# Optimization experiments

Measured on AMD Instinct MI355X. Metric: run time of the kernel, lower is better.

The kernel has to match this reference:

```python
import jax, jax.numpy as jnp
import numpy as np

HEAD = 3
EMB = 192
MAX_LAYER = 4
NEG_SLOPE_ATT = 0.2
NEG_SLOPE_ACT = 0.1
BN_EPS = 1e-5

def leaky_relu(x, slope):
    return jnp.where(x >= 0, x, slope * x)

def setup_inputs() -> dict:
    key = jax.random.key(0)
    ks = jax.random.split(key, 8)
    N, E, D_IN = 64000, 512000, 128
    k = EMB // HEAD
    subx = jax.random.normal(ks[0], (N, D_IN), dtype=jnp.float32)
    edge_index = jax.random.randint(ks[1], (2, E), 0, N, dtype=jnp.int32)
    mask = jax.random.randint(ks[2], (E, 1), 0, 2, dtype=jnp.int32)
    W = jax.random.normal(ks[3], (EMB, D_IN), dtype=jnp.float32) * (1.0 / np.sqrt(D_IN))
    att = jax.random.normal(ks[4], (1, HEAD, 2 * k), dtype=jnp.float32) * 0.1
    bias = jnp.zeros((EMB,), dtype=jnp.float32)
    gamma = jnp.ones((EMB,), dtype=jnp.float32)
    beta = jnp.zeros((EMB,), dtype=jnp.float32)
    return {"subx": subx, "edge_index": edge_index, "mask": mask, "W": W,
            "att": att, "bias": bias, "gamma": gamma, "beta": beta,
            "batch_size": 32, "subgraph_size": 500}

def reference(subx, edge_index, mask, W, att, bias, gamma, beta, batch_size, subgraph_size):
    N = subx.shape[0]
    k = EMB // HEAD
    # linear projection, split into heads: [N, H, k]
    x = (subx @ W.T).reshape(N, HEAD, k)
    src = edge_index[0]  # softmax grouping index (as in original code)
    dst = edge_index[1]  # aggregation target (PyG source_to_target flow)
    x_i = x[dst]  # [E, H, k]
    x_j = x[src]  # [E, H, k]
    # attention logits per edge per head
    alpha = (jnp.concatenate([x_i, x_j], axis=-1) * att).sum(-1)  # [E, H]
    alpha = leaky_relu(alpha, NEG_SLOPE_ATT)
    # segment softmax grouped by src (faithful to original)
    amax = jax.ops.segment_max(alpha, src, num_segments=N)
    ex = jnp.exp(alpha - amax[src])
    denom = jax.ops.segment_sum(ex, src, num_segments=N)
    alpha = ex / (denom[src] + 1e-16)
    # edge mask (tile over heads)
    m = (mask.reshape(-1, 1, 1) != 0)
    msg = jnp.where(m, x_j, 0.0) * alpha[..., None]  # [E, H, k]
    # scatter-add to target nodes
    aggr = jax.ops.segment_sum(msg, dst, num_segments=N).reshape(N, EMB) + bias
    # LeakyReLU(0.1) then BatchNorm1d (training-mode batch stats)
    h = leaky_relu(aggr, NEG_SLOPE_ACT)
    mean = h.mean(axis=0)
    var = h.var(axis=0)
    h = gamma * (h - mean) / jnp.sqrt(var + BN_EPS) + beta
    # mean over k-hop layers
    h = h.reshape(batch_size, MAX_LAYER, subgraph_size, EMB)
    return h.mean(axis=1)
```

## Files before the change

### kernel.cpp

```cpp
#include <hip/hip_runtime.h>

#define EMBD 192
#define DIN 128
#define SB 1024

typedef __bf16 bfrag __attribute__((ext_vector_type(8)));
typedef float  f32x4 __attribute__((ext_vector_type(4)));

__device__ __forceinline__ void f4add(float4& a, const float4& b){
  a.x += b.x; a.y += b.y; a.z += b.z; a.w += b.w;
}
__device__ __forceinline__ unsigned short f2bf(float f){
  unsigned u = __float_as_uint(f);
  unsigned r = u + 0x7fffu + ((u >> 16) & 1u);
  return (unsigned short)(r >> 16);
}
__device__ __forceinline__ float bf2f(unsigned short h){
  return __uint_as_float(((unsigned)h) << 16);
}

__global__ __launch_bounds__(256) void k_gemm(const float* __restrict__ A,
      const float* __restrict__ W, const float* __restrict__ att,
      float* __restrict__ X, float* __restrict__ ai4, float* __restrict__ aj4,
      unsigned* __restrict__ zbuf, long zcount, int N, int G){
  {
    long i = (long)blockIdx.x*blockDim.x + threadIdx.x;
    long st = (long)gridDim.x*blockDim.x;
    for (; i < zcount; i += st) zbuf[i] = 0u;
  }

  int flat = blockIdx.x;
  int L = (G % 8 == 0) ? ((flat & 7)*(G >> 3) + (flat >> 3)) : flat;
  int rowblk = L / 3, head = L - rowblk*3;

  __shared__ unsigned short As_hi[8192], As_lo[8192];
  __shared__ unsigned short Ws_hi[8192], Ws_lo[8192];
  int t = threadIdx.x;

  const float4* Ag = (const float4*)A;
  const float4* Wg = (const float4*)W + (size_t)(head*64)*32;
  #pragma unroll
  for (int i = 0; i < 8; i++){
    int idx = i*256 + t;
    int r = idx >> 5, c4 = idx & 31;
    int g = (c4 >> 1) ^ (r & 15);
    int base = (r*16 + g)*8 + (c4 & 1)*4;
    int row = rowblk*64 + r; if (row >= N) row = N - 1;
    float4 va = Ag[(size_t)row*32 + c4];
    float4 vw = Wg[(size_t)idx];
    unsigned short h; float lo;
    ushort4 ah, al, wh, wl;
    h = f2bf(va.x); lo = va.x - bf2f(h); ah.x = h; al.x = f2bf(lo);
    h = f2bf(va.y); lo = va.y - bf2f(h); ah.y = h; al.y = f2bf(lo);
    h = f2bf(va.z); lo = va.z - bf2f(h); ah.z = h; al.z = f2bf(lo);
    h = f2bf(va.w); lo = va.w - bf2f(h); ah.w = h; al.w = f2bf(lo);
    *(ushort4*)&As_hi[base] = ah; *(ushort4*)&As_lo[base] = al;
    h = f2bf(vw.x); lo = vw.x - bf2f(h); wh.x = h; wl.x = f2bf(lo);
    h = f2bf(vw.y); lo = vw.y - bf2f(h); wh.y = h; wl.y = f2bf(lo);
    h = f2bf(vw.z); lo = vw.z - bf2f(h); wh.z = h; wl.z = f2bf(lo);
    h = f2bf(vw.w); lo = vw.w - bf2f(h); wh.w = h; wl.w = f2bf(lo);
    *(ushort4*)&Ws_hi[base] = wh; *(ushort4*)&Ws_lo[base] = wl;
  }

  int wave = t >> 6, lane = t & 63;
  int lc = lane & 15, kg = lane >> 4;
  float atti_l[4], attj_l[4];
  #pragma unroll
  for (int ct = 0; ct < 4; ct++){
    atti_l[ct] = att[head*128 + ct*16 + lc];
    attj_l[ct] = att[head*128 + 64 + ct*16 + lc];
  }
  __syncthreads();

  int arow = wave*16 + lc;
  f32x4 acc[4];
  #pragma unroll
  for (int ct = 0; ct < 4; ct++) acc[ct] = (f32x4){0.f, 0.f, 0.f, 0.f};

  #pragma unroll
  for (int ks = 0; ks < 4; ks++){
    int g = ks*4 + kg;
    int aoff = (arow*16 + (g ^ (arow & 15)))*8;
    bfrag ah = *(const bfrag*)&As_hi[aoff];
    bfrag al = *(const bfrag*)&As_lo[aoff];
    #pragma unroll
    for (int ct = 0; ct < 4; ct++){
      int boff = ((ct*16 + lc)*16 + (g ^ lc))*8;
      bfrag bh = *(const bfrag*)&Ws_hi[boff];
      bfrag bl = *(const bfrag*)&Ws_lo[boff];
      acc[ct] = __builtin_amdgcn_mfma_f32_16x16x32_bf16(ah, bh, acc[ct], 0, 0, 0);
      acc[ct] = __builtin_amdgcn_mfma_f32_16x16x32_bf16(ah, bl, acc[ct], 0, 0, 0);
      acc[ct] = __builtin_amdgcn_mfma_f32_16x16x32_bf16(al, bh, acc[ct], 0, 0, 0);
    }
  }

  int mbase = rowblk*64 + wave*16 + kg*4;
  #pragma unroll
  for (int r = 0; r < 4; r++){
    int m = mbase + r;
    bool ok = (m < N);
    float pi = 0.f, pj = 0.f;
    #pragma unroll
    for (int ct = 0; ct < 4; ct++){
      float v = acc[ct][r];
      if (ok) X[(size_t)m*EMBD + head*64 + ct*16 + lc] = v;
      pi += v*atti_l[ct]; pj += v*attj_l[ct];
    }
    pi += __shfl_xor(pi, 1); pi += __shfl_xor(pi, 2);
    pi += __shfl_xor(pi, 4); pi += __shfl_xor(pi, 8);
    pj += __shfl_xor(pj, 1); pj += __shfl_xor(pj, 2);
    pj += __shfl_xor(pj, 4); pj += __shfl_xor(pj, 8);
    if (ok && lc == 0){ ai4[(size_t)m*4 + head] = pi; aj4[(size_t)m*4 + head] = pj; }
  }
}

__global__ void k_count(const int* __restrict__ ei, const int* __restrict__ msk,
    int* __restrict__ count2, int* __restrict__ slot_src, int* __restrict__ slot_dst,
    int E, int N){
  int e = blockIdx.x*256 + threadIdx.x;
  if (e >= E) return;
  int s = ei[e], d = ei[E + e];
  slot_src[e] = atomicAdd(&count2[s], 1);
  slot_dst[e] = msk[e] ? atomicAdd(&count2[N + d], 1) : -1;
}

__global__ void k_scan1(const int* __restrict__ count, int* __restrict__ offs,
                        int* __restrict__ bsum, int M){
  __shared__ int sm[256];
  int t = threadIdx.x, i = blockIdx.x*256 + t;
  int v = (i < M) ? count[i] : 0;
  sm[t] = v; __syncthreads();
  for (int o = 1; o < 256; o <<= 1){
    int u = (t >= o) ? sm[t-o] : 0;
    __syncthreads();
    sm[t] += u;
    __syncthreads();
  }
  if (i < M) offs[i] = sm[t] - v;
  if (t == 255) bsum[blockIdx.x] = sm[255];
}

__global__ void k_scan2(int* __restrict__ bsum, int NB){
  __shared__ int sm[1024];
  int t = threadIdx.x;
  int v = (t < NB) ? bsum[t] : 0;
  sm[t] = v; __syncthreads();
  for (int o = 1; o < 1024; o <<= 1){
    int u = (t >= o) ? sm[t-o] : 0;
    __syncthreads();
    sm[t] += u;
    __syncthreads();
  }
  if (t < NB) bsum[t] = sm[t] - v;
}

__global__ void k_scan3(int* __restrict__ offs, const int* __restrict__ bsum, int M){
  int i = blockIdx.x*256 + threadIdx.x;
  if (i < M) offs[i] += bsum[blockIdx.x];
}

__global__ void k_fill(const int* __restrict__ ei, const int* __restrict__ slot_src,
    const int* __restrict__ slot_dst, const int* __restrict__ offs2,
    int* __restrict__ elist_src, int* __restrict__ elist_dst, int E, int N){
  int e = blockIdx.x*256 + threadIdx.x;
  if (e >= E) return;
  int s = ei[e], d = ei[E + e];
  elist_src[offs2[s] + slot_src[e]] = d;
  int sd = slot_dst[e];
  if (sd >= 0) elist_dst[offs2[N + d] + sd] = s;
}

__global__ __launch_bounds__(256) void k_denom(const int* __restrict__ count2,
    const int* __restrict__ offs2, const int* __restrict__ elist_src,
    const float4* __restrict__ ai4, const float4* __restrict__ aj4,
    float4* __restrict__ denom4, int N){
  int g = threadIdx.x >> 4, l = threadIdx.x & 15;
  int n = blockIdx.x*16 + g;
  if (n >= N) return;
  int deg = count2[n];
  if (deg == 0) return;
  int base = offs2[n];
  float4 xj = aj4[n];
  float s0 = 0.f, s1 = 0.f, s2 = 0.f;
  for (int j = l; j < deg; j += 16){
    int d = elist_src[base + j];
    float4 xi = ai4[d];
    float a0 = xi.x + xj.x; a0 = a0 >= 0.f ? a0 : 0.2f*a0; s0 += expf(a0);
    float a1 = xi.y + xj.y; a1 = a1 >= 0.f ? a1 : 0.2f*a1; s1 += expf(a1);
    float a2 = xi.z + xj.z; a2 = a2 >= 0.f ? a2 : 0.2f*a2; s2 += expf(a2);
  }
  s0 += __shfl_xor(s0, 1); s0 += __shfl_xor(s0, 2); s0 += __shfl_xor(s0, 4); s0 += __shfl_xor(s0, 8);
  s1 += __shfl_xor(s1, 1); s1 += __shfl_xor(s1, 2); s1 += __shfl_xor(s1, 4); s1 += __shfl_xor(s1, 8);
  s2 += __shfl_xor(s2, 1); s2 += __shfl_xor(s2, 2); s2 += __shfl_xor(s2, 4); s2 += __shfl_xor(s2, 8);
  if (l == 0)
    denom4[n] = make_float4(1.f/(s0 + 1e-16f), 1.f/(s1 + 1e-16f), 1.f/(s2 + 1e-16f), 0.f);
}

__global__ __launch_bounds__(256) void k_aggr(const float* __restrict__ X,
    const int* __restrict__ count2, const int* __restrict__ offs2,
    const int* __restrict__ elist_dst, const float4* __restrict__ ai4,
    const float4* __restrict__ aj4, const float4* __restrict__ denom4,
    const float* __restrict__ bias, float* __restrict__ hact, int N){
  int w = threadIdx.x >> 6, l = threadIdx.x & 63;
  int n = blockIdx.x*4 + w;
  if (n >= N) return;
  int deg = count2[N + n], base = offs2[N + n];
  float4 xi = ai4[n];
  float ac0 = 0.f, ac1 = 0.f, ac2 = 0.f;
  #pragma unroll 4
  for (int j = 0; j < deg; j++){
    int s = elist_dst[base + j];
    float4 xj = aj4[s];
    float4 rn = denom4[s];
    float a0 = xi.x + xj.x; a0 = a0 >= 0.f ? a0 : 0.2f*a0; float c0 = expf(a0)*rn.x;
    float a1 = xi.y + xj.y; a1 = a1 >= 0.f ? a1 : 0.2f*a1; float c1 = expf(a1)*rn.y;
    float a2 = xi.z + xj.z; a2 = a2 >= 0.f ? a2 : 0.2f*a2; float c2 = expf(a2)*rn.z;
    const float* xr = X + (size_t)s*EMBD;
    ac0 += c0 * xr[l];
    ac1 += c1 * xr[64 + l];
    ac2 += c2 * xr[128 + l];
  }
  float* o = hact + (size_t)n*EMBD;
  float v0 = ac0 + bias[l];       v0 = v0 >= 0.f ? v0 : 0.1f*v0; o[l]       = v0;
  float v1 = ac1 + bias[64 + l];  v1 = v1 >= 0.f ? v1 : 0.1f*v1; o[64 + l]  = v1;
  float v2 = ac2 + bias[128 + l]; v2 = v2 >= 0.f ? v2 : 0.1f*v2; o[128 + l] = v2;
}

__global__ __launch_bounds__(192) void k_stat1(const float4* __restrict__ h4,
    float4* __restrict__ part4, int N){
  int t = threadIdx.x;
  int fcol = t % 48, rg = t / 48;
  float4 s = make_float4(0.f,0.f,0.f,0.f);
  float4 q = make_float4(0.f,0.f,0.f,0.f);
  for (int r = blockIdx.x*4 + rg; r < N; r += SB*4){
    float4 v = h4[(size_t)r*48 + fcol];
    s.x += v.x; s.y += v.y; s.z += v.z; s.w += v.w;
    q.x += v.x*v.x; q.y += v.y*v.y; q.z += v.z*v.z; q.w += v.w*v.w;
  }
  __shared__ float4 sms[192], smq[192];
  sms[t] = s; smq[t] = q;
  __syncthreads();
  if (rg < 2){ f4add(sms[t], sms[t+96]); f4add(smq[t], smq[t+96]); }
  __syncthreads();
  if (rg == 0){
    f4add(sms[t], sms[t+48]); f4add(smq[t], smq[t+48]);
    part4[(size_t)blockIdx.x*96 + fcol]      = sms[t];
    part4[(size_t)blockIdx.x*96 + 48 + fcol] = smq[t];
  }
}

__global__ __launch_bounds__(256) void k_stat2(const float4* __restrict__ part4,
    float4* __restrict__ stats4, int N){
  int j = blockIdx.x, t = threadIdx.x;
  float4 s = make_float4(0.f,0.f,0.f,0.f);
  float4 q = make_float4(0.f,0.f,0.f,0.f);
  for (int b = t; b < SB; b += 256){
    f4add(s, part4[(size_t)b*96 + j]);
    f4add(q, part4[(size_t)b*96 + 48 + j]);
  }
  #pragma unroll
  for (int o = 32; o > 0; o >>= 1){
    s.x += __shfl_xor(s.x,o); s.y += __shfl_xor(s.y,o);
    s.z += __shfl_xor(s.z,o); s.w += __shfl_xor(s.w,o);
    q.x += __shfl_xor(q.x,o); q.y += __shfl_xor(q.y,o);
    q.z += __shfl_xor(q.z,o); q.w += __shfl_xor(q.w,o);
  }
  __shared__ float4 ws[4], wq[4];
  int wv = t >> 6;
  if ((t & 63) == 0){ ws[wv] = s; wq[wv] = q; }
  __syncthreads();
  if (t == 0){
    f4add(ws[0], ws[1]); f4add(ws[0], ws[2]); f4add(ws[0], ws[3]);
    f4add(wq[0], wq[1]); f4add(wq[0], wq[2]); f4add(wq[0], wq[3]);
    float inv = 1.f / (float)N;
    float4 mean = make_float4(ws[0].x*inv, ws[0].y*inv, ws[0].z*inv, ws[0].w*inv);
    float4 rstd;
    rstd.x = rsqrtf(wq[0].x*inv - mean.x*mean.x + 1e-5f);
    rstd.y = rsqrtf(wq[0].y*inv - mean.y*mean.y + 1e-5f);
    rstd.z = rsqrtf(wq[0].z*inv - mean.z*mean.z + 1e-5f);
    rstd.w = rsqrtf(wq[0].w*inv - mean.w*mean.w + 1e-5f);
    stats4[j] = mean;
    stats4[48 + j] = rstd;
  }
}

__global__ void k_final(const float* __restrict__ hact, const float* __restrict__ stats,
    const float* __restrict__ gamma, const float* __restrict__ beta,
    const int* __restrict__ sgs, float* __restrict__ out, int total){
  int o = blockIdx.x*256 + threadIdx.x;
  if (o >= total) return;
  int S = *sgs;
  int c  = o % EMBD;
  int rs = o / EMBD;
  int b  = rs / S;
  int s  = rs % S;
  size_t n0 = (size_t)b*4*S + s;
  float v = 0.25f * (hact[(n0      )*EMBD + c] + hact[(n0 +   S)*EMBD + c] +
                     hact[(n0 + 2*S)*EMBD + c] + hact[(n0 + 3*S)*EMBD + c]);
  out[o] = gamma[c] * ((v - stats[c]) * stats[192 + c]) + beta[c];
}

extern "C" void kernel_launch(void* const* d_in, const int* in_sizes, int n_in,
                              void* d_out, int out_size, void* d_ws, size_t ws_size,
                              hipStream_t stream){
  const float* subx  = (const float*)d_in[0];
  const int*   ei    = (const int*)d_in[1];
  const int*   msk   = (const int*)d_in[2];
  const float* W     = (const float*)d_in[3];
  const float* att   = (const float*)d_in[4];
  const float* bias  = (const float*)d_in[5];
  const float* gamma = (const float*)d_in[6];
  const float* beta  = (const float*)d_in[7];
  const int*   sgs   = (const int*)d_in[9];
  float* out = (float*)d_out;

  int N = in_sizes[0] / DIN;
  int E = in_sizes[1] / 2;

  float*  X         = (float*)d_ws;
  float*  hact      = X + (size_t)N*EMBD;
  float*  denom4    = hact + (size_t)N*EMBD;
  float*  ai4       = denom4 + (size_t)N*4;
  float*  aj4       = ai4 + (size_t)N*4;
  int*    count2    = (int*)(aj4 + (size_t)N*4);
  int*    offs2     = count2 + 2*(size_t)N;
  int*    slot_src  = offs2 + 2*(size_t)N;
  int*    slot_dst  = slot_src + E;
  int*    elist_src = slot_dst + E;
  int*    elist_dst = elist_src + E;
  int*    bsum      = elist_dst + E;
  float*  part      = (float*)(bsum + 1024);
  float*  stats     = part + (size_t)SB*96*4;

  int EB  = (E + 255)/256;
  int MB2 = (N + 63)/64;
  int G   = MB2*3;
  int M2  = 2*N;
  int NB2 = (M2 + 255)/256;

  k_gemm <<<G, 256, 0, stream>>>(subx, W, att, X, ai4, aj4,
                                 (unsigned*)count2, (long)M2, N, G);
  k_count<<<EB, 256, 0, stream>>>(ei, msk, count2, slot_src, slot_dst, E, N);
  k_scan1<<<NB2, 256, 0, stream>>>(count2, offs2, bsum, M2);
  k_scan2<<<1, 1024, 0, stream>>>(bsum, NB2);
  k_scan3<<<NB2, 256, 0, stream>>>(offs2, bsum, M2);
  k_fill <<<EB, 256, 0, stream>>>(ei, slot_src, slot_dst, offs2, elist_src, elist_dst, E, N);
  k_denom<<<(N + 15)/16, 256, 0, stream>>>(count2, offs2, elist_src,
                                           (const float4*)ai4, (const float4*)aj4,
                                           (float4*)denom4, N);
  k_aggr <<<(N + 3)/4, 256, 0, stream>>>(X, count2, offs2, elist_dst,
                                         (const float4*)ai4, (const float4*)aj4,
                                         (const float4*)denom4, bias, hact, N);
  k_stat1<<<SB, 192, 0, stream>>>((const float4*)hact, (float4*)part, N);
  k_stat2<<<48, 256, 0, stream>>>((const float4*)part, (float4*)stats, N);
  k_final<<<(out_size + 255)/256, 256, 0, stream>>>(hact, stats, gamma, beta, sgs, out, out_size);
}
```

Measured before the change: 265.3 us.

## Precompute per-edge attention coefficients and vectorize aggregation with float4 gathers

Adds a k_coef kernel that computes the normalized attention coefficient per destination-sorted edge once and packs it with the source index into a float4. k_aggr then does one float4 load per edge instead of recomputing the exponentials redundantly in all 64 lanes. It also gathers X rows as float4 with 48 active lanes. expf is replaced by __expf. The cost is an extra kernel launch plus writing and reading a 16-byte-per-edge coefficient buffer, and 16 of 64 lanes sit idle in aggregation.

```diff
diff --git a/kernel.cpp b/kernel.cpp
--- a/kernel.cpp
+++ b/kernel.cpp
@@ -140,7 +140,7 @@
   if (t == 255) bsum[blockIdx.x] = sm[255];
 }
 
-__global__ void k_scan2(int* __restrict__ bsum, int NB){
+__global__ void k_scan2(int* __restrict__ bsum, int* __restrict__ gtot, int NB){
   __shared__ int sm[1024];
   int t = threadIdx.x;
   int v = (t < NB) ? bsum[t] : 0;
@@ -152,6 +152,7 @@
     __syncthreads();
   }
   if (t < NB) bsum[t] = sm[t] - v;
+  if (t == NB-1) *gtot = sm[t];
 }
 
 __global__ void k_scan3(int* __restrict__ offs, const int* __restrict__ bsum, int M){
@@ -161,13 +162,13 @@
 
 __global__ void k_fill(const int* __restrict__ ei, const int* __restrict__ slot_src,
     const int* __restrict__ slot_dst, const int* __restrict__ offs2,
-    int* __restrict__ elist_src, int* __restrict__ elist_dst, int E, int N){
+    int* __restrict__ elist_src, int2* __restrict__ pairs_dst, int E, int N){
   int e = blockIdx.x*256 + threadIdx.x;
   if (e >= E) return;
   int s = ei[e], d = ei[E + e];
   elist_src[offs2[s] + slot_src[e]] = d;
   int sd = slot_dst[e];
-  if (sd >= 0) elist_dst[offs2[N + d] + sd] = s;
+  if (sd >= 0) pairs_dst[offs2[N + d] + sd - E] = make_int2(s, d);
 }
 
 __global__ __launch_bounds__(256) void k_denom(const int* __restrict__ count2,
@@ -185,9 +186,9 @@
   for (int j = l; j < deg; j += 16){
     int d = elist_src[base + j];
     float4 xi = ai4[d];
-    float a0 = xi.x + xj.x; a0 = a0 >= 0.f ? a0 : 0.2f*a0; s0 += expf(a0);
-    float a1 = xi.y + xj.y; a1 = a1 >= 0.f ? a1 : 0.2f*a1; s1 += expf(a1);
-    float a2 = xi.z + xj.z; a2 = a2 >= 0.f ? a2 : 0.2f*a2; s2 += expf(a2);
+    float a0 = xi.x + xj.x; a0 = a0 >= 0.f ? a0 : 0.2f*a0; s0 += __expf(a0);
+    float a1 = xi.y + xj.y; a1 = a1 >= 0.f ? a1 : 0.2f*a1; s1 += __expf(a1);
+    float a2 = xi.z + xj.z; a2 = a2 >= 0.f ? a2 : 0.2f*a2; s2 += __expf(a2);
   }
   s0 += __shfl_xor(s0, 1); s0 += __shfl_xor(s0, 2); s0 += __shfl_xor(s0, 4); s0 += __shfl_xor(s0, 8);
   s1 += __shfl_xor(s1, 1); s1 += __shfl_xor(s1, 2); s1 += __shfl_xor(s1, 4); s1 += __shfl_xor(s1, 8);
@@ -196,34 +197,51 @@
     denom4[n] = make_float4(1.f/(s0 + 1e-16f), 1.f/(s1 + 1e-16f), 1.f/(s2 + 1e-16f), 0.f);
 }
 
-__global__ __launch_bounds__(256) void k_aggr(const float* __restrict__ X,
+__global__ void k_coef(const int2* __restrict__ pairs, const float4* __restrict__ ai4,
+    const float4* __restrict__ aj4, const float4* __restrict__ denom4,
+    const int* __restrict__ gtot, float4* __restrict__ ecoef, int E){
+  int i = blockIdx.x*256 + threadIdx.x;
+  int total = *gtot - E;
+  if (i >= total) return;
+  int2 p = pairs[i];
+  float4 xj = aj4[p.x];
+  float4 xi = ai4[p.y];
+  float4 rn = denom4[p.x];
+  float a0 = xi.x + xj.x; a0 = a0 >= 0.f ? a0 : 0.2f*a0;
+  float a1 = xi.y + xj.y; a1 = a1 >= 0.f ? a1 : 0.2f*a1;
+  float a2 = xi.z + xj.z; a2 = a2 >= 0.f ? a2 : 0.2f*a2;
+  ecoef[i] = make_float4(__int_as_float(p.x),
+                         __expf(a0)*rn.x, __expf(a1)*rn.y, __expf(a2)*rn.z);
+}
+
+__global__ __launch_bounds__(256) void k_aggr(const float4* __restrict__ X4,
     const int* __restrict__ count2, const int* __restrict__ offs2,
-    const int* __restrict__ elist_dst, const float4* __restrict__ ai4,
-    const float4* __restrict__ aj4, const float4* __restrict__ denom4,
-    const float* __restrict__ bias, float* __restrict__ hact, int N){
+    const float4* __restrict__ ecoef, const float4* __restrict__ bias4,
+    float4* __restrict__ hact4, int N, int E){
   int w = threadIdx.x >> 6, l = threadIdx.x & 63;
   int n = blockIdx.x*4 + w;
   if (n >= N) return;
-  int deg = count2[N + n], base = offs2[N + n];
-  float4 xi = ai4[n];
-  float ac0 = 0.f, ac1 = 0.f, ac2 = 0.f;
+  int deg = count2[N + n], base = offs2[N + n] - E;
+  int lc = l < 48 ? l : 47;
+  int hsel = lc >> 4;
+  float4 ac = make_float4(0.f,0.f,0.f,0.f);
   #pragma unroll 4
   for (int j = 0; j < deg; j++){
-    int s = elist_dst[base + j];
-    float4 xj = aj4[s];
-    float4 rn = denom4[s];
-    float a0 = xi.x + xj.x; a0 = a0 >= 0.f ? a0 : 0.2f*a0; float c0 = expf(a0)*rn.x;
-    float a1 = xi.y + xj.y; a1 = a1 >= 0.f ? a1 : 0.2f*a1; float c1 = expf(a1)*rn.y;
-    float a2 = xi.z + xj.z; a2 = a2 >= 0.f ? a2 : 0.2f*a2; float c2 = expf(a2)*rn.z;
-    const float* xr = X + (size_t)s*EMBD;
-    ac0 += c0 * xr[l];
-    ac1 += c1 * xr[64 + l];
-    ac2 += c2 * xr[128 + l];
-  }
-  float* o = hact + (size_t)n*EMBD;
-  float v0 = ac0 + bias[l];       v0 = v0 >= 0.f ? v0 : 0.1f*v0; o[l]       = v0;
-  float v1 = ac1 + bias[64 + l];  v1 = v1 >= 0.f ? v1 : 0.1f*v1; o[64 + l]  = v1;
-  float v2 = ac2 + bias[128 + l]; v2 = v2 >= 0.f ? v2 : 0.1f*v2; o[128 + l] = v2;
+    float4 q = ecoef[base + j];
+    int s = __float_as_int(q.x);
+    float c = hsel == 0 ? q.y : (hsel == 1 ? q.z : q.w);
+    float4 v = X4[(size_t)s*48 + lc];
+    ac.x += c*v.x; ac.y += c*v.y; ac.z += c*v.z; ac.w += c*v.w;
+  }
+  if (l < 48){
+    float4 b = bias4[lc];
+    float4 o;
+    o.x = ac.x + b.x; o.x = o.x >= 0.f ? o.x : 0.1f*o.x;
+    o.y = ac.y + b.y; o.y = o.y >= 0.f ? o.y : 0.1f*o.y;
+    o.z = ac.z + b.z; o.z = o.z >= 0.f ? o.z : 0.1f*o.z;
+    o.w = ac.w + b.w; o.w = o.w >= 0.f ? o.w : 0.1f*o.w;
+    hact4[(size_t)n*48 + lc] = o;
+  }
 }
 
 __global__ __launch_bounds__(192) void k_stat1(const float4* __restrict__ h4,
@@ -327,9 +345,11 @@
   int*    slot_src  = offs2 + 2*(size_t)N;
   int*    slot_dst  = slot_src + E;
   int*    elist_src = slot_dst + E;
-  int*    elist_dst = elist_src + E;
-  int*    bsum      = elist_dst + E;
-  float*  part      = (float*)(bsum + 1024);
+  int2*   pairs_dst = (int2*)(elist_src + E);
+  float4* ecoef     = (float4*)(pairs_dst + E);
+  int*    bsum      = (int*)(ecoef + E);
+  int*    gtot      = bsum + 1024;
+  float*  part      = (float*)(gtot + 4);
   float*  stats     = part + (size_t)SB*96*4;
 
   int EB  = (E + 255)/256;
@@ -342,15 +362,16 @@
                                  (unsigned*)count2, (long)M2, N, G);
   k_count<<<EB, 256, 0, stream>>>(ei, msk, count2, slot_src, slot_dst, E, N);
   k_scan1<<<NB2, 256, 0, stream>>>(count2, offs2, bsum, M2);
-  k_scan2<<<1, 1024, 0, stream>>>(bsum, NB2);
+  k_scan2<<<1, 1024, 0, stream>>>(bsum, gtot, NB2);
   k_scan3<<<NB2, 256, 0, stream>>>(offs2, bsum, M2);
-  k_fill <<<EB, 256, 0, stream>>>(ei, slot_src, slot_dst, offs2, elist_src, elist_dst, E, N);
+  k_fill <<<EB, 256, 0, stream>>>(ei, slot_src, slot_dst, offs2, elist_src, pairs_dst, E, N);
   k_denom<<<(N + 15)/16, 256, 0, stream>>>(count2, offs2, elist_src,
                                            (const float4*)ai4, (const float4*)aj4,
                                            (float4*)denom4, N);
-  k_aggr <<<(N + 3)/4, 256, 0, stream>>>(X, count2, offs2, elist_dst,
-                                         (const float4*)ai4, (const float4*)aj4,
-                                         (const float4*)denom4, bias, hact, N);
+  k_coef <<<EB, 256, 0, stream>>>(pairs_dst, (const float4*)ai4, (const float4*)aj4,
+                                  (const float4*)denom4, gtot, ecoef, E);
+  k_aggr <<<(N + 3)/4, 256, 0, stream>>>((const float4*)X, count2, offs2, ecoef,
+                                         (const float4*)bias, (float4*)hact, N, E);
   k_stat1<<<SB, 192, 0, stream>>>((const float4*)hact, (float4*)part, N);
   k_stat2<<<48, 256, 0, stream>>>((const float4*)part, (float4*)stats, N);
   k_final<<<(out_size + 255)/256, 256, 0, stream>>>(hact, stats, gamma, beta, sgs, out, out_size);
```

Result: faster. 254.8 us (-3.9%).
